# Performance work log

Measured on AMD Instinct MI355X. Metric: run time of the kernel, lower is better.

Reference implementation:

```python
import jax, jax.numpy as jnp
import numpy as np

B, S, D_IN, D_H = 4, 2048, 1024, 1024

def setup_inputs() -> dict:
    key = jax.random.key(0)
    kx, kq, kk, kv = jax.random.split(key, 4)
    # nn.Linear default init: U(-1/sqrt(fan_in), 1/sqrt(fan_in)); stored as [out, in]
    bound = 1.0 / np.sqrt(D_IN)
    x = jax.random.normal(kx, (B, S, D_IN), dtype=jnp.float32)
    W_q = jax.random.uniform(kq, (D_H, D_IN), jnp.float32, -bound, bound)
    W_k = jax.random.uniform(kk, (D_H, D_IN), jnp.float32, -bound, bound)
    W_v = jax.random.uniform(kv, (D_H, D_IN), jnp.float32, -bound, bound)
    return {"x": x, "W_q": W_q, "W_k": W_k, "W_v": W_v}

def reference(x, W_q, W_k, W_v):
    # Q = x @ W_q.T, etc. (nn.Linear with bias=False)
    Q = jnp.einsum('bsd,hd->bsh', x, W_q)
    K = jnp.einsum('bsd,hd->bsh', x, W_k)
    V = jnp.einsum('bsd,hd->bsh', x, W_v)
    # NOTE: original scales by sqrt(Q.shape[1]) == sqrt(seq_len), not sqrt(d)
    scale = 1.0 / jnp.sqrt(jnp.asarray(Q.shape[1], Q.dtype))
    scores = jnp.einsum('bqh,bkh->bqk', Q, K) * scale  # [B,S,S]
    attn = jax.nn.softmax(scores, axis=-1)
    return jnp.einsum('bqk,bkh->bqh', attn, V)
```

## Files before the change

### kernel.cpp

```cpp
#include <hip/hip_runtime.h>

typedef unsigned short ushort_t;
typedef __attribute__((ext_vector_type(8))) __bf16 bf16x8;
typedef __attribute__((ext_vector_type(4))) float floatx4;

__device__ __forceinline__ ushort_t f2bf(float f) {
    unsigned int u = __builtin_bit_cast(unsigned int, f);
    u = (u + 0x7fffu + ((u >> 16) & 1u)) >> 16;
    return (ushort_t)u;
}

__device__ __forceinline__ void async16(const ushort_t* g, ushort_t* l) {
    __builtin_amdgcn_global_load_lds(
        (const __attribute__((address_space(1))) unsigned int*)g,
        (__attribute__((address_space(3))) unsigned int*)l,
        16 , 0 , 0 );
}

__device__ __forceinline__ int sw(int row, int cg) {
    return ((row << 2) + ((cg ^ row ^ (row >> 2)) & 3)) << 3;
}

template <int BM, int BN, int IM, int IN, int NW>
__device__ __forceinline__ void gemm_core_p3(
    const ushort_t* __restrict__ A, int lda,
    const ushort_t* __restrict__ B, int ldb,
    int K, int tile_m, int tile_n,
    ushort_t* buf,
    floatx4 (&acc)[IM][IN]) {

    constexpr int NT = NW * 64;
    constexpr int SA = BM * 4 / NT;
    constexpr int SB = BN * 4 / NT;
    constexpr int SLOT = (BM + BN) * 32;
    constexpr int BOFF = BM * 32;

    const int tid  = threadIdx.x;
    const int lane = tid & 63;
    const int wave = tid >> 6;
    const int wm   = wave >> 1, wn = wave & 1;
    const int quad = lane >> 4;
    const int l16  = lane & 15;

#pragma unroll
    for (int i = 0; i < IM; i++)
#pragma unroll
        for (int j = 0; j < IN; j++) acc[i][j] = (floatx4){0.f, 0.f, 0.f, 0.f};

    const ushort_t* ga[SA];
    int la[SA];
#pragma unroll
    for (int s = 0; s < SA; s++) {
        int seg = tid + s * NT;
        int r = seg >> 2, c = (seg ^ r ^ (r >> 2)) & 3;
        ga[s] = A + (long)(r + tile_m) * lda + c * 8;
        la[s] = seg * 8;
    }
    const ushort_t* gb[SB];
    int lb[SB];
#pragma unroll
    for (int s = 0; s < SB; s++) {
        int seg = tid + s * NT;
        int r = seg >> 2, c = (seg ^ r ^ (r >> 2)) & 3;
        gb[s] = B + (long)(r + tile_n) * ldb + c * 8;
        lb[s] = BOFF + seg * 8;
    }

    const int nk = K >> 5;

#pragma unroll
    for (int p = 0; p < 2; ++p) {
#pragma unroll
        for (int s = 0; s < SA; s++) async16(ga[s] + p * 32, buf + p * SLOT + la[s]);
#pragma unroll
        for (int s = 0; s < SB; s++) async16(gb[s] + p * 32, buf + p * SLOT + lb[s]);
    }

    int slot = 0, slot2 = 2;
    for (int k = 0; k < nk; ++k) {
        if (k + 1 < nk) {
            if constexpr (SA + SB == 4)
                asm volatile("s_waitcnt vmcnt(4)" ::: "memory");
            else if constexpr (SA + SB == 3)
                asm volatile("s_waitcnt vmcnt(3)" ::: "memory");
            else
                asm volatile("s_waitcnt vmcnt(2)" ::: "memory");
        } else {
            asm volatile("s_waitcnt vmcnt(0)" ::: "memory");
        }
        __builtin_amdgcn_s_barrier();
        asm volatile("" ::: "memory");

        if (k + 2 < nk) {
            const int koff = (k + 2) << 5;
            ushort_t* dst = buf + slot2 * SLOT;
#pragma unroll
            for (int s = 0; s < SA; s++) async16(ga[s] + koff, dst + la[s]);
#pragma unroll
            for (int s = 0; s < SB; s++) async16(gb[s] + koff, dst + lb[s]);
        }

        const ushort_t* as = buf + slot * SLOT;
        const ushort_t* bs = as + BOFF;
        bf16x8 af[IM], bfr[IN];
#pragma unroll
        for (int im = 0; im < IM; im++)
            af[im] = *(const bf16x8*)&as[sw(wm * IM * 16 + im * 16 + l16, quad)];
#pragma unroll
        for (int in = 0; in < IN; in++)
            bfr[in] = *(const bf16x8*)&bs[sw(wn * IN * 16 + in * 16 + l16, quad)];
#pragma unroll
        for (int im = 0; im < IM; im++)
#pragma unroll
            for (int in = 0; in < IN; in++)
                acc[im][in] = __builtin_amdgcn_mfma_f32_16x16x32_bf16(
                    af[im], bfr[in], acc[im][in], 0, 0, 0);

        slot  = (slot == 2) ? 0 : slot + 1;
        slot2 = (slot2 == 2) ? 0 : slot2 + 1;
    }
}

__global__ void prep_kernel(const float* __restrict__ x,
                            const float* __restrict__ wq,
                            const float* __restrict__ wk,
                            const float* __restrict__ wv,
                            ushort_t* __restrict__ xb,
                            ushort_t* __restrict__ wvb,
                            ushort_t* __restrict__ wqT,
                            ushort_t* __restrict__ wkT,
                            float* __restrict__ lsum) {
    const int bx = blockIdx.x;
    const int t = threadIdx.x;
    if (bx < 9216) {
        const float* src;
        ushort_t* dst;
        long g;
        if (bx < 8192) { src = x;  dst = xb;  g = ((long)bx * 256 + t) * 4; }
        else           { src = wv; dst = wvb; g = ((long)(bx - 8192) * 256 + t) * 4; }
        float4 v = *(const float4*)(src + g);
        ushort4 o;
        o.x = f2bf(v.x); o.y = f2bf(v.y); o.z = f2bf(v.z); o.w = f2bf(v.w);
        *(ushort4*)(dst + g) = o;
        return;
    }
    if (bx < 9224) {
        int idx = (bx - 9216) * 256 + t;
        ((float4*)lsum)[idx] = (float4){0.f, 0.f, 0.f, 0.f};
        return;
    }
    const int tt = bx - 9224;
    const float* src = (tt >= 256) ? wk : wq;
    ushort_t* dst = (tt >= 256) ? wkT : wqT;
    const int id = tt & 255;
    const int h0 = (id >> 4) * 64, d0 = (id & 15) * 64;
    __shared__ ushort_t tile[64 * 80];
    {
        int i = t >> 2, cg = (t & 3) << 4;
        const float4* p = (const float4*)(src + (long)(h0 + i) * 1024 + d0 + cg);
#pragma unroll
        for (int k = 0; k < 4; k++) {
            float4 v = p[k];
            ushort_t* q = &tile[i * 80 + cg + k * 4];
            q[0] = f2bf(v.x); q[1] = f2bf(v.y); q[2] = f2bf(v.z); q[3] = f2bf(v.w);
        }
    }
    __syncthreads();
    {
        int j = t >> 2, ig = (t & 3) << 4;
        ushort_t tmp[16];
#pragma unroll
        for (int k = 0; k < 16; k++) tmp[k] = tile[(ig + k) * 80 + j];
        ushort_t* o = dst + (long)(d0 + j) * 1024 + h0 + ig;
        *(uint4*)o = ((uint4*)tmp)[0];
        *(uint4*)(o + 8) = ((uint4*)tmp)[1];
    }
}

__global__ __launch_bounds__(512, 4) void gv_kernel(
    const ushort_t* __restrict__ wkT, const ushort_t* __restrict__ wqT,
    const ushort_t* __restrict__ wvb, const ushort_t* __restrict__ xb,
    ushort_t* __restrict__ Gb, ushort_t* __restrict__ VTb) {

    __shared__ __align__(16) ushort_t buf[3 * 384 * 32];

    const ushort_t *A, *B;
    ushort_t* C;
    int ldc, tile_m, tile_n;
    if (blockIdx.x < 32) {
        A = wkT; B = wqT; C = Gb; ldc = 1024;
        tile_m = (blockIdx.x >> 3) * 256;
        tile_n = (blockIdx.x & 7) * 128;
    } else {
        int id = blockIdx.x - 32;
        A = wvb; B = xb; C = VTb; ldc = 8192;
        tile_m = (id >> 6) * 256;
        tile_n = (id & 63) * 128;
    }

    floatx4 acc[4][4];
    gemm_core_p3<256, 128, 4, 4, 8>(A, 1024, B, 1024, 1024, tile_m, tile_n, buf, acc);

    const int lane = threadIdx.x & 63, wave = threadIdx.x >> 6;
    const int wm = wave >> 1, wn = wave & 1, quad = lane >> 4, l16 = lane & 15;
#pragma unroll
    for (int im = 0; im < 4; im++)
#pragma unroll
        for (int r = 0; r < 4; r++) {
            int row = tile_m + wm * 64 + im * 16 + quad * 4 + r;
#pragma unroll
            for (int in = 0; in < 4; in++) {
                int col = tile_n + wn * 64 + in * 16 + l16;
                C[(long)row * ldc + col] = f2bf(acc[im][in][r]);
            }
        }
}

__global__ __launch_bounds__(256) void y_kernel(
    const ushort_t* __restrict__ xb,
    const ushort_t* __restrict__ Gb,
    ushort_t* __restrict__ Yb) {

    __shared__ __align__(16) ushort_t buf[3 * 256 * 32];
    const int tile_m = blockIdx.y * 128;
    const int tile_n = blockIdx.x * 128;

    floatx4 acc[4][4];
    gemm_core_p3<128, 128, 4, 4, 4>(xb, 1024, Gb, 1024, 1024, tile_m, tile_n, buf, acc);

    const int lane = threadIdx.x & 63, wave = threadIdx.x >> 6;
    const int wm = wave >> 1, wn = wave & 1, quad = lane >> 4, l16 = lane & 15;
#pragma unroll
    for (int im = 0; im < 4; im++)
#pragma unroll
        for (int r = 0; r < 4; r++) {
            int row = tile_m + wm * 64 + im * 16 + quad * 4 + r;
#pragma unroll
            for (int in = 0; in < 4; in++) {
                int col = tile_n + wn * 64 + in * 16 + l16;
                Yb[(long)row * 1024 + col] = f2bf(acc[im][in][r]);
            }
        }
}

__global__ __launch_bounds__(512, 4) void pexp_kernel(
    const ushort_t* __restrict__ Yb,
    const ushort_t* __restrict__ xb,
    ushort_t* __restrict__ Pb,
    float* __restrict__ lsum) {

    __shared__ __align__(16) ushort_t buf[3 * 384 * 32];

    const int z = blockIdx.z;
    const ushort_t* A = Yb + (long)z * 2097152;
    const ushort_t* B = xb + (long)z * 2097152;
    ushort_t* C = Pb + (long)z * 4194304;
    float* l = lsum + z * 2048;
    const int tile_m = blockIdx.y * 256;
    const int tile_n = blockIdx.x * 128;

    floatx4 acc[4][4];
    gemm_core_p3<256, 128, 4, 4, 8>(A, 1024, B, 1024, 1024, tile_m, tile_n, buf, acc);

    const float scale = 0.022097086912079608f;
    const int lane = threadIdx.x & 63, wave = threadIdx.x >> 6;
    const int wm = wave >> 1, wn = wave & 1, quad = lane >> 4, l16 = lane & 15;
#pragma unroll
    for (int im = 0; im < 4; im++)
#pragma unroll
        for (int r = 0; r < 4; r++) {
            int row = tile_m + wm * 64 + im * 16 + quad * 4 + r;
            float psum = 0.f;
#pragma unroll
            for (int in = 0; in < 4; in++) {
                int col = tile_n + wn * 64 + in * 16 + l16;
                float e = __expf(acc[im][in][r] * scale);
                C[(long)row * 2048 + col] = f2bf(e);
                psum += e;
            }
            psum += __shfl_xor(psum, 1, 64);
            psum += __shfl_xor(psum, 2, 64);
            psum += __shfl_xor(psum, 4, 64);
            psum += __shfl_xor(psum, 8, 64);
            if (l16 == 0) atomicAdd(&l[row], psum);
        }
}

__global__ __launch_bounds__(256) void out_kernel(
    const ushort_t* __restrict__ Pb,
    const ushort_t* __restrict__ VTb,
    float* __restrict__ out,
    const float* __restrict__ lsum) {

    __shared__ __align__(16) ushort_t buf[3 * 256 * 32];

    const int z = blockIdx.z;
    const ushort_t* A = Pb + (long)z * 4194304;
    const ushort_t* B = VTb + (long)z * 2048;
    float* C = out + (long)z * 2097152;
    const float* l = lsum + z * 2048;
    const int tile_m = blockIdx.y * 128;
    const int tile_n = blockIdx.x * 128;

    floatx4 acc[4][4];
    gemm_core_p3<128, 128, 4, 4, 4>(A, 2048, B, 8192, 2048, tile_m, tile_n, buf, acc);

    const int lane = threadIdx.x & 63, wave = threadIdx.x >> 6;
    const int wm = wave >> 1, wn = wave & 1, quad = lane >> 4, l16 = lane & 15;
#pragma unroll
    for (int im = 0; im < 4; im++)
#pragma unroll
        for (int r = 0; r < 4; r++) {
            int row = tile_m + wm * 64 + im * 16 + quad * 4 + r;
            float li = 1.0f / l[row];
#pragma unroll
            for (int in = 0; in < 4; in++) {
                int col = tile_n + wn * 64 + in * 16 + l16;
                C[(long)row * 1024 + col] = acc[im][in][r] * li;
            }
        }
}

extern "C" void kernel_launch(void* const* d_in, const int* in_sizes, int n_in,
                              void* d_out, int out_size, void* d_ws, size_t ws_size,
                              hipStream_t stream) {
    const float* x  = (const float*)d_in[0];
    const float* wq = (const float*)d_in[1];
    const float* wk = (const float*)d_in[2];
    const float* wv = (const float*)d_in[3];

    ushort_t* xb  = (ushort_t*)d_ws;
    ushort_t* wvb = xb  + 8388608;
    ushort_t* wqT = wvb + 1048576;
    ushort_t* wkT = wqT + 1048576;
    ushort_t* Gb  = wkT + 1048576;
    ushort_t* Yb  = Gb  + 1048576;
    ushort_t* VTb = Yb  + 8388608;
    ushort_t* Pb  = VTb + 8388608;
    float*    lsum = (float*)(Pb + 16777216);
    float*    out  = (float*)d_out;

    prep_kernel<<<9736, 256, 0, stream>>>(x, wq, wk, wv, xb, wvb, wqT, wkT, lsum);

    gv_kernel<<<288, 512, 0, stream>>>(wkT, wqT, wvb, xb, Gb, VTb);

    y_kernel<<<dim3(8, 64), 256, 0, stream>>>(xb, Gb, Yb);

    pexp_kernel<<<dim3(16, 8, 4), 512, 0, stream>>>(Yb, xb, Pb, lsum);

    out_kernel<<<dim3(8, 16, 4), 256, 0, stream>>>(Pb, VTb, out, lsum);
}
```

Baseline: 241.2 us.

## Add XCD-aware block swizzle and 4-stage LDS pipeline for 128x128 GEMMs

Generalizes the GEMM core to a configurable number of LDS pipeline stages and uses four stages for the y and out kernels. It also flattens their grids to 1D and remaps block IDs so that consecutive tiles land on the same XCD, improving L2 reuse of shared A/B panels. The deeper pipeline increases LDS use per block, which may reduce occupancy.

```diff
diff --git a/kernel.cpp b/kernel.cpp
--- a/kernel.cpp
+++ b/kernel.cpp
@@ -21,8 +21,22 @@
     return ((row << 2) + ((cg ^ row ^ (row >> 2)) & 3)) << 3;
 }
 
-template <int BM, int BN, int IM, int IN, int NW>
-__device__ __forceinline__ void gemm_core_p3(
+__device__ __forceinline__ int xcd_swz(int bid, int cpx) {
+    return (bid & 7) * cpx + (bid >> 3);
+}
+
+template <int N>
+__device__ __forceinline__ void vwait() {
+    if constexpr (N == 0)      asm volatile("s_waitcnt vmcnt(0)" ::: "memory");
+    else if constexpr (N == 3) asm volatile("s_waitcnt vmcnt(3)" ::: "memory");
+    else if constexpr (N == 4) asm volatile("s_waitcnt vmcnt(4)" ::: "memory");
+    else if constexpr (N == 6) asm volatile("s_waitcnt vmcnt(6)" ::: "memory");
+    else if constexpr (N == 8) asm volatile("s_waitcnt vmcnt(8)" ::: "memory");
+    else static_assert(N == 0, "unsupported vmcnt");
+}
+
+template <int BM, int BN, int IM, int IN, int NW, int NS>
+__device__ __forceinline__ void gemm_core_p(
     const ushort_t* __restrict__ A, int lda,
     const ushort_t* __restrict__ B, int ldb,
     int K, int tile_m, int tile_n,
@@ -32,6 +46,7 @@
     constexpr int NT = NW * 64;
     constexpr int SA = BM * 4 / NT;
     constexpr int SB = BN * 4 / NT;
+    constexpr int Q  = SA + SB;
     constexpr int SLOT = (BM + BN) * 32;
     constexpr int BOFF = BM * 32;
 
@@ -69,30 +84,28 @@
     const int nk = K >> 5;
 
 #pragma unroll
-    for (int p = 0; p < 2; ++p) {
+    for (int p = 0; p < NS - 1; ++p) {
 #pragma unroll
         for (int s = 0; s < SA; s++) async16(ga[s] + p * 32, buf + p * SLOT + la[s]);
 #pragma unroll
         for (int s = 0; s < SB; s++) async16(gb[s] + p * 32, buf + p * SLOT + lb[s]);
     }
 
-    int slot = 0, slot2 = 2;
+    int slot = 0, slot2 = NS - 1;
     for (int k = 0; k < nk; ++k) {
-        if (k + 1 < nk) {
-            if constexpr (SA + SB == 4)
-                asm volatile("s_waitcnt vmcnt(4)" ::: "memory");
-            else if constexpr (SA + SB == 3)
-                asm volatile("s_waitcnt vmcnt(3)" ::: "memory");
-            else
-                asm volatile("s_waitcnt vmcnt(2)" ::: "memory");
+        const int rem = nk - 1 - k;
+        if (rem >= NS - 2) {
+            vwait<(NS - 2) * Q>();
+        } else if (NS >= 4 && rem == 1) {
+            vwait<Q>();
         } else {
-            asm volatile("s_waitcnt vmcnt(0)" ::: "memory");
+            vwait<0>();
         }
         __builtin_amdgcn_s_barrier();
         asm volatile("" ::: "memory");
 
-        if (k + 2 < nk) {
-            const int koff = (k + 2) << 5;
+        if (k + NS - 1 < nk) {
+            const int koff = (k + NS - 1) << 5;
             ushort_t* dst = buf + slot2 * SLOT;
 #pragma unroll
             for (int s = 0; s < SA; s++) async16(ga[s] + koff, dst + la[s]);
@@ -116,8 +129,8 @@
                 acc[im][in] = __builtin_amdgcn_mfma_f32_16x16x32_bf16(
                     af[im], bfr[in], acc[im][in], 0, 0, 0);
 
-        slot  = (slot == 2) ? 0 : slot + 1;
-        slot2 = (slot2 == 2) ? 0 : slot2 + 1;
+        slot  = (slot == NS - 1) ? 0 : slot + 1;
+        slot2 = (slot2 == NS - 1) ? 0 : slot2 + 1;
     }
 }
 
@@ -199,7 +212,7 @@
     }
 
     floatx4 acc[4][4];
-    gemm_core_p3<256, 128, 4, 4, 8>(A, 1024, B, 1024, 1024, tile_m, tile_n, buf, acc);
+    gemm_core_p<256, 128, 4, 4, 8, 3>(A, 1024, B, 1024, 1024, tile_m, tile_n, buf, acc);
 
     const int lane = threadIdx.x & 63, wave = threadIdx.x >> 6;
     const int wm = wave >> 1, wn = wave & 1, quad = lane >> 4, l16 = lane & 15;
@@ -221,12 +234,13 @@
     const ushort_t* __restrict__ Gb,
     ushort_t* __restrict__ Yb) {
 
-    __shared__ __align__(16) ushort_t buf[3 * 256 * 32];
-    const int tile_m = blockIdx.y * 128;
-    const int tile_n = blockIdx.x * 128;
+    __shared__ __align__(16) ushort_t buf[4 * 256 * 32];
+    const int lin = xcd_swz(blockIdx.x, 64);
+    const int tile_n = (lin & 7) * 128;
+    const int tile_m = (lin >> 3) * 128;
 
     floatx4 acc[4][4];
-    gemm_core_p3<128, 128, 4, 4, 4>(xb, 1024, Gb, 1024, 1024, tile_m, tile_n, buf, acc);
+    gemm_core_p<128, 128, 4, 4, 4, 4>(xb, 1024, Gb, 1024, 1024, tile_m, tile_n, buf, acc);
 
     const int lane = threadIdx.x & 63, wave = threadIdx.x >> 6;
     const int wm = wave >> 1, wn = wave & 1, quad = lane >> 4, l16 = lane & 15;
@@ -251,16 +265,18 @@
 
     __shared__ __align__(16) ushort_t buf[3 * 384 * 32];
 
-    const int z = blockIdx.z;
+    const int lin = xcd_swz(blockIdx.x, 64);
+    const int z = lin >> 7;
+    const int tile_m = ((lin >> 4) & 7) * 256;
+    const int tile_n = (lin & 15) * 128;
+
     const ushort_t* A = Yb + (long)z * 2097152;
     const ushort_t* B = xb + (long)z * 2097152;
     ushort_t* C = Pb + (long)z * 4194304;
     float* l = lsum + z * 2048;
-    const int tile_m = blockIdx.y * 256;
-    const int tile_n = blockIdx.x * 128;
 
     floatx4 acc[4][4];
-    gemm_core_p3<256, 128, 4, 4, 8>(A, 1024, B, 1024, 1024, tile_m, tile_n, buf, acc);
+    gemm_core_p<256, 128, 4, 4, 8, 3>(A, 1024, B, 1024, 1024, tile_m, tile_n, buf, acc);
 
     const float scale = 0.022097086912079608f;
     const int lane = threadIdx.x & 63, wave = threadIdx.x >> 6;
@@ -292,18 +308,20 @@
     float* __restrict__ out,
     const float* __restrict__ lsum) {
 
-    __shared__ __align__(16) ushort_t buf[3 * 256 * 32];
-
-    const int z = blockIdx.z;
+    __shared__ __align__(16) ushort_t buf[4 * 256 * 32];
+
+    const int lin = xcd_swz(blockIdx.x, 64);
+    const int z = lin >> 7;
+    const int tile_m = ((lin >> 3) & 15) * 128;
+    const int tile_n = (lin & 7) * 128;
+
     const ushort_t* A = Pb + (long)z * 4194304;
     const ushort_t* B = VTb + (long)z * 2048;
     float* C = out + (long)z * 2097152;
     const float* l = lsum + z * 2048;
-    const int tile_m = blockIdx.y * 128;
-    const int tile_n = blockIdx.x * 128;
 
     floatx4 acc[4][4];
-    gemm_core_p3<128, 128, 4, 4, 4>(A, 2048, B, 8192, 2048, tile_m, tile_n, buf, acc);
+    gemm_core_p<128, 128, 4, 4, 4, 4>(A, 2048, B, 8192, 2048, tile_m, tile_n, buf, acc);
 
     const int lane = threadIdx.x & 63, wave = threadIdx.x >> 6;
     const int wm = wave >> 1, wn = wave & 1, quad = lane >> 4, l16 = lane & 15;
@@ -344,9 +362,9 @@
 
     gv_kernel<<<288, 512, 0, stream>>>(wkT, wqT, wvb, xb, Gb, VTb);
 
-    y_kernel<<<dim3(8, 64), 256, 0, stream>>>(xb, Gb, Yb);
-
-    pexp_kernel<<<dim3(16, 8, 4), 512, 0, stream>>>(Yb, xb, Pb, lsum);
-
-    out_kernel<<<dim3(8, 16, 4), 256, 0, stream>>>(Pb, VTb, out, lsum);
-}
+    y_kernel<<<512, 256, 0, stream>>>(xb, Gb, Yb);
+
+    pexp_kernel<<<512, 512, 0, stream>>>(Yb, xb, Pb, lsum);
+
+    out_kernel<<<512, 256, 0, stream>>>(Pb, VTb, out, lsum);
+}
```

Result: faster. 229.2 us (-5.0%).
